# Performance work log

Measured on AMD Instinct MI355X. Metric: run time of the kernel, lower is better.

## Reference

```python
import jax, jax.numpy as jnp
import numpy as np

B_, T_, N_ = 32, 96, 68
IN_F, HID, GRU_H, NCLS = 3, 128, 128, 10
DEG = 8
N_NODES = B_ * T_ * N_
N_EDGES = N_NODES * DEG


def setup_inputs() -> dict:
    key = jax.random.key(0)
    ks = jax.random.split(key, 16)
    s = 0.05
    rn = lambda k, shp: (jax.random.normal(k, shp, jnp.float32) * s)
    return {
        "x": jax.random.normal(ks[0], (N_NODES, IN_F), jnp.float32),
        "edge_index": jax.random.randint(ks[1], (2, N_EDGES), 0, N_NODES, jnp.int32),
        "W_gcn0": rn(ks[2], (IN_F, HID)),
        "b_gcn0": jnp.zeros((HID,), jnp.float32),
        "W_gcn1": rn(ks[3], (HID, HID)),
        "b_gcn1": jnp.zeros((HID,), jnp.float32),
        "W_mlp": rn(ks[4], (HID, HID)),
        "b_mlp": jnp.zeros((HID,), jnp.float32),
        "W_ih": rn(ks[5], (3 * GRU_H, HID)),
        "W_hh": rn(ks[6], (3 * GRU_H, GRU_H)),
        "b_ih": jnp.zeros((3 * GRU_H,), jnp.float32),
        "b_hh": jnp.zeros((3 * GRU_H,), jnp.float32),
        "W_c1": rn(ks[7], (GRU_H, GRU_H // 2)),
        "b_c1": jnp.zeros((GRU_H // 2,), jnp.float32),
        "W_c2": rn(ks[8], (GRU_H // 2, NCLS)),
        "b_c2": jnp.zeros((NCLS,), jnp.float32),
        "B": B_, "T": T_, "N": N_,
    }


def reference(x, edge_index, W_gcn0, b_gcn0, W_gcn1, b_gcn1, W_mlp, b_mlp,
              W_ih, W_hh, b_ih, b_hh, W_c1, b_c1, W_c2, b_c2, B, T, N):
    n_nodes = x.shape[0]
    src, dst = edge_index[0], edge_index[1]
    # GCN degree with self-loops: deg[i] = 1 + in-degree(i)
    deg = jnp.ones((n_nodes,), x.dtype).at[dst].add(1.0)
    d_isqrt = jax.lax.rsqrt(deg)
    self_norm = (d_isqrt * d_isqrt)[:, None]  # self-loop norm = 1/deg
    edge_norm = (d_isqrt[src] * d_isqrt[dst])[:, None]

    def gcn(h, W, b):
        h = h @ W
        agg = jax.ops.segment_sum(h[src] * edge_norm, dst, num_segments=n_nodes)
        return agg + h * self_norm + b

    h = jax.nn.relu(gcn(x, W_gcn0, b_gcn0))
    h = jax.nn.relu(gcn(h, W_gcn1, b_gcn1))
    h = jax.nn.relu(h @ W_mlp + b_mlp)  # node_mlp (dropout off in eval)

    frames = h.reshape(B, T, N, -1).mean(axis=2)  # [B, T, HID] frame pooling

    def gru_step(hs, xt):
        gi = xt @ W_ih.T + b_ih
        gh = hs @ W_hh.T + b_hh
        ir, iz, inn = jnp.split(gi, 3, axis=-1)
        hr, hz, hn = jnp.split(gh, 3, axis=-1)
        r = jax.nn.sigmoid(ir + hr)
        z = jax.nn.sigmoid(iz + hz)
        n_new = jnp.tanh(inn + r * hn)
        return (1.0 - z) * n_new + z * hs, None

    h0 = jnp.zeros((B, GRU_H), frames.dtype)
    hT, _ = jax.lax.scan(gru_step, h0, jnp.swapaxes(frames, 0, 1))

    hidden = jax.nn.relu(hT @ W_c1 + b_c1)
    return hidden @ W_c2 + b_c2  # logits [B, num_classes]
```

## Files before the change

kernel.cpp:

```cpp
#include <hip/hip_runtime.h>

#define NN_TOT 208896
#define E_TOT  1671168
#define B_SZ   32
#define T_SZ   96
#define NPF    68
#define HID    128
#define NBINS  204
#define CAP    9216
#define NSB    816

typedef _Float16 f16x8 __attribute__((ext_vector_type(8)));
typedef _Float16 f16x2v __attribute__((ext_vector_type(2)));
typedef float f32x4 __attribute__((ext_vector_type(4)));

__global__ __launch_bounds__(256) void k_scatter(const int* __restrict__ src, const int* __restrict__ dst,
                                                 int* __restrict__ gcur, int2* __restrict__ er_tmp,
                                                 const float* __restrict__ Wih, const float* __restrict__ Whh,
                                                 const float* __restrict__ W1, const float* __restrict__ Wm,
                                                 const float* __restrict__ W0, const float* __restrict__ b0,
                                                 _Float16* __restrict__ Wihh, _Float16* __restrict__ Wihl,
                                                 _Float16* __restrict__ W1p, _Float16* __restrict__ Wmp,
                                                 _Float16* __restrict__ Whhp, _Float16* __restrict__ W0h,
                                                 _Float16* __restrict__ b0h) {
    const int bid = blockIdx.x;
    const int tid = threadIdx.x;
    if (bid >= NSB) {
        int i = (bid - NSB) * 256 + tid;
        {
            int e = i & 7;
            int lane = (i >> 3) & 63;
            int f = i >> 9;
            int j = f >> 2, kk = f & 3;
            int q = lane >> 4, p = lane & 15;
            float wv = Wih[(size_t)(j * 16 + p) * 128 + kk * 32 + q * 8 + e];
            _Float16 hi = (_Float16)wv;
            Wihh[i] = hi;
            Wihl[i] = (_Float16)(wv - (float)hi);
        }
        {
            int e = i & 7;
            int lane = (i >> 3) & 63;
            int f = i >> 9;
            int kk = f & 3, g = (f >> 2) % 3, wv = f / 12;
            int q = lane >> 4, c = lane & 15;
            Whhp[i] = (_Float16)Whh[(size_t)(g * 128 + 16 * wv + c) * 128 + kk * 32 + q * 8 + e];
        }
        if (i < 16384) {
            int f = i >> 9;
            int j = f >> 2, kk = f & 3;
            int lane = (i >> 3) & 63;
            int e = i & 7;
            int q = lane >> 4, p = lane & 15;
            int k = kk * 32 + q * 8 + e, n = j * 16 + p;
            W1p[i] = (_Float16)W1[k * 128 + n];
            Wmp[i] = (_Float16)Wm[k * 128 + n];
        }
        if (i < 384) W0h[i] = (_Float16)W0[i];
        if (i < 128) b0h[i] = (_Float16)b0[i];
        return;
    }
    __shared__ int hist[NBINS];
    __shared__ int lbase[NBINS];
    for (int i = tid; i < NBINS; i += 256) hist[i] = 0;
    __syncthreads();
    const int be = bid * 2048 + tid * 8;
    int s[8], d[8], rk[8];
    *(int4*)&s[0] = *(const int4*)&src[be];
    *(int4*)&s[4] = *(const int4*)&src[be + 4];
    *(int4*)&d[0] = *(const int4*)&dst[be];
    *(int4*)&d[4] = *(const int4*)&dst[be + 4];
#pragma unroll
    for (int j = 0; j < 8; ++j) rk[j] = atomicAdd(&hist[d[j] >> 10], 1);
    __syncthreads();
    for (int i = tid; i < NBINS; i += 256) lbase[i] = atomicAdd(&gcur[i], hist[i]);
    __syncthreads();
#pragma unroll
    for (int j = 0; j < 8; ++j) {
        int b = d[j] >> 10;
        er_tmp[(size_t)b * CAP + lbase[b] + rk[j]] = make_int2(s[j], d[j]);
    }
}

__global__ __launch_bounds__(256) void k_binsort2(const int2* __restrict__ er_tmp, const int* __restrict__ gcur,
                                                  const float* __restrict__ x, int* __restrict__ er,
                                                  int2* __restrict__ row2, float4* __restrict__ xd) {
    __shared__ int lcnt[1024];
    __shared__ int lofs[1024];
    __shared__ int ts[256];
    const int tid = threadIdx.x;
    const int nb = blockIdx.x << 10;
    const int base0 = blockIdx.x * CAP;
    for (int i = tid; i < 1024; i += 256) lcnt[i] = 0;
    __syncthreads();
    const int end = base0 + gcur[blockIdx.x];
    for (int e = base0 + tid; e < end; e += 256) {
        int2 ed = er_tmp[e];
        atomicAdd(&lcnt[ed.y - nb], 1);
    }
    __syncthreads();
    const int base = tid * 4;
    const int c0 = lcnt[base], c1 = lcnt[base + 1], c2 = lcnt[base + 2], c3 = lcnt[base + 3];
    int ssum = c0 + c1 + c2 + c3;
    ts[tid] = ssum;
    __syncthreads();
    int inc = ssum;
    for (int off = 1; off < 256; off <<= 1) {
        int add = (tid >= off) ? ts[tid - off] : 0;
        __syncthreads();
        inc += add;
        ts[tid] = inc;
        __syncthreads();
    }
    const int b0 = base0 + (inc - ssum);
    lofs[base] = b0;
    lofs[base + 1] = b0 + c0;
    lofs[base + 2] = b0 + c0 + c1;
    lofs[base + 3] = b0 + c0 + c1 + c2;
    row2[nb + base] = make_int2(b0, b0 + c0);
    row2[nb + base + 1] = make_int2(b0 + c0, b0 + c0 + c1);
    row2[nb + base + 2] = make_int2(b0 + c0 + c1, b0 + c0 + c1 + c2);
    row2[nb + base + 3] = make_int2(b0 + c0 + c1 + c2, b0 + ssum);
    {
        const float4* xv = (const float4*)(x + 3 * (size_t)(nb + base));
        float4 a = xv[0], b = xv[1], c = xv[2];
        float i0 = 1.0f / sqrtf(1.f + (float)c0);
        float i1 = 1.0f / sqrtf(1.f + (float)c1);
        float i2 = 1.0f / sqrtf(1.f + (float)c2);
        float i3 = 1.0f / sqrtf(1.f + (float)c3);
        xd[nb + base + 0] = make_float4(a.x * i0, a.y * i0, a.z * i0, i0);
        xd[nb + base + 1] = make_float4(a.w * i1, b.x * i1, b.y * i1, i1);
        xd[nb + base + 2] = make_float4(b.z * i2, b.w * i2, c.x * i2, i2);
        xd[nb + base + 3] = make_float4(c.y * i3, c.z * i3, c.w * i3, i3);
    }
    __syncthreads();
    for (int e = base0 + tid; e < end; e += 256) {
        int2 ed = er_tmp[e];
        int p = atomicAdd(&lofs[ed.y - nb], 1);
        er[p] = ed.x;
    }
}

__global__ __launch_bounds__(256) void k_z0(const float4* __restrict__ xd, const int2* __restrict__ row2,
                                            const int* __restrict__ er, float4* __restrict__ z0out) {
    const int tid = threadIdx.x;
    const int blk = blockIdx.x;
    const int li = tid >> 2;
    const int slot = tid & 3;
    const int n = blk * 64 + li;
    const int2 be2 = row2[n];
    float p0 = 0.f, p1 = 0.f, p2 = 0.f;
    for (int ei = be2.x + slot; ei < be2.y; ei += 4) {
        float4 f = xd[er[ei]];
        p0 += f.x;
        p1 += f.y;
        p2 += f.z;
    }
    p0 += __shfl_xor(p0, 1); p1 += __shfl_xor(p1, 1); p2 += __shfl_xor(p2, 1);
    p0 += __shfl_xor(p0, 2); p1 += __shfl_xor(p1, 2); p2 += __shfl_xor(p2, 2);
    if (slot == 0) {
        const float4 own = xd[n];
        const float w = own.w;
        float4 z;
        z.x = w * (p0 + own.x);
        z.y = w * (p1 + own.y);
        z.z = w * (p2 + own.z);
        z.w = w;
        z0out[n] = z;
    }
}

__global__ __launch_bounds__(256, 4) void k_agg_mm(const float4* __restrict__ z0, const int2* __restrict__ row2,
                                                   const int* __restrict__ er, const _Float16* __restrict__ W0h,
                                                   const _Float16* __restrict__ b0h, const _Float16* __restrict__ W1p,
                                                   const float* __restrict__ b1, _Float16* __restrict__ h1) {
    __shared__ __align__(16) _Float16 As[64 * 136];
    const int tid = threadIdx.x;
    const int w = tid >> 6, lane = tid & 63;
    const int blk = blockIdx.x;

    {
        const int node = blk * 64 + lane;
        const int2 be2 = row2[node];
        const int beg = be2.x, end = be2.y;
        const f16x2v* __restrict__ W0p = (const f16x2v*)W0h;
        const f16x2v* __restrict__ b0p = (const f16x2v*)b0h;
        const int pb = w * 16;
        const f16x2v zero2 = {(_Float16)0.f, (_Float16)0.f};
        f16x2v w0p[16], w1p[16], w2p[16], bbp[16];
#pragma unroll
        for (int j = 0; j < 16; ++j) {
            w0p[j] = W0p[pb + j];
            w1p[j] = W0p[64 + pb + j];
            w2p[j] = W0p[128 + pb + j];
            bbp[j] = b0p[pb + j];
        }
        const float4 zs = z0[node];
        const _Float16 isd = (_Float16)zs.w;
        const f16x2v dnn = {isd, isd};
        f16x2v accp[16];
        {
            _Float16 sx = (_Float16)zs.x, sy = (_Float16)zs.y, sz = (_Float16)zs.z;
            f16x2v zxx = {sx, sx}, zyy = {sy, sy}, zzz = {sz, sz};
#pragma unroll
            for (int j = 0; j < 16; ++j) {
                f16x2v t = zxx * w0p[j] + (zyy * w1p[j] + (zzz * w2p[j] + bbp[j]));
                t = __builtin_elementwise_max(t, zero2);
                accp[j] = t * dnn;
            }
        }
        int ei = beg;
        for (; ei + 2 <= end; ei += 2) {
            int sa = er[ei], sb = er[ei + 1];
            float4 za = z0[sa];
            float4 zb = z0[sb];
            _Float16 ax = (_Float16)za.x, ay = (_Float16)za.y, az = (_Float16)za.z;
            _Float16 aen = (_Float16)za.w;
            _Float16 bx = (_Float16)zb.x, by = (_Float16)zb.y, bz = (_Float16)zb.z;
            _Float16 ben = (_Float16)zb.w;
            f16x2v axx = {ax, ax}, ayy = {ay, ay}, azz = {az, az}, aee = {aen, aen};
            f16x2v bxx = {bx, bx}, byy = {by, by}, bzz = {bz, bz}, bee = {ben, ben};
#pragma unroll
            for (int j = 0; j < 16; ++j) {
                f16x2v t = axx * w0p[j] + (ayy * w1p[j] + (azz * w2p[j] + bbp[j]));
                t = __builtin_elementwise_max(t, zero2);
                accp[j] = t * aee + accp[j];
            }
#pragma unroll
            for (int j = 0; j < 16; ++j) {
                f16x2v t = bxx * w0p[j] + (byy * w1p[j] + (bzz * w2p[j] + bbp[j]));
                t = __builtin_elementwise_max(t, zero2);
                accp[j] = t * bee + accp[j];
            }
        }
        if (ei < end) {
            float4 za = z0[er[ei]];
            _Float16 ax = (_Float16)za.x, ay = (_Float16)za.y, az = (_Float16)za.z;
            _Float16 aen = (_Float16)za.w;
            f16x2v axx = {ax, ax}, ayy = {ay, ay}, azz = {az, az}, aee = {aen, aen};
#pragma unroll
            for (int j = 0; j < 16; ++j) {
                f16x2v t = axx * w0p[j] + (ayy * w1p[j] + (azz * w2p[j] + bbp[j]));
                t = __builtin_elementwise_max(t, zero2);
                accp[j] = t * aee + accp[j];
            }
        }
        _Float16* dst = &As[lane * 136 + w * 32];
#pragma unroll
        for (int j = 0; j < 16; ++j) *(f16x2v*)(dst + 2 * j) = accp[j] * dnn;
    }
    __syncthreads();

    const int q = lane >> 4, c = lane & 15;
    f16x8 afr[4];
#pragma unroll
    for (int kk = 0; kk < 4; ++kk) afr[kk] = *(const f16x8*)(&As[(w * 16 + c) * 136 + kk * 32 + q * 8]);
    const f16x8* __restrict__ Bv = (const f16x8*)W1p;
    _Float16* Cst = &As[w * 2176];
#pragma unroll
    for (int j = 0; j < 8; ++j) {
        f32x4 cc = {0.f, 0.f, 0.f, 0.f};
#pragma unroll
        for (int kk = 0; kk < 4; ++kk)
            cc = __builtin_amdgcn_mfma_f32_16x16x32_f16(afr[kk], Bv[(j * 4 + kk) * 64 + lane], cc, 0, 0, 0);
        const float bi = b1[j * 16 + c];
#pragma unroll
        for (int r = 0; r < 4; ++r) Cst[(q * 4 + r) * 128 + j * 16 + c] = (_Float16)fmaxf(cc[r] + bi, 0.f);
    }
#pragma unroll
    for (int it = 0; it < 4; ++it) {
        int idx = it * 64 + lane;
        *(f16x8*)(h1 + (size_t)(blk * 64 + w * 16) * 128 + idx * 8) = *(const f16x8*)(&As[w * 2176 + idx * 8]);
    }
}

__global__ __launch_bounds__(256) void k_mm_pool(const _Float16* __restrict__ h1, const _Float16* __restrict__ Wmp,
                                                 const float* __restrict__ bm, _Float16* __restrict__ FRh,
                                                 _Float16* __restrict__ FRl) {
    __shared__ __align__(16) _Float16 As[80 * 136];
    __shared__ float colpart[4 * 128];
    const int tid = threadIdx.x;
    const int w = tid >> 6, lane = tid & 63;
    const int q = lane >> 4, c = lane & 15;
    const int bt = blockIdx.x;

    const f16x8* __restrict__ srcv = (const f16x8*)(h1 + (size_t)bt * NPF * HID);
    for (int idx = tid; idx < 80 * 17; idx += 256) {
        int row = idx / 17, ch = idx % 17;
        f16x8 v;
        if (row < NPF && ch < 16) {
            v = srcv[row * 16 + ch];
        } else {
#pragma unroll
            for (int k = 0; k < 8; ++k) v[k] = (_Float16)0.f;
        }
        *(f16x8*)(&As[row * 136 + ch * 8]) = v;
    }
    __syncthreads();

    const f16x8* __restrict__ Bv = (const f16x8*)Wmp;
    const int npass = (w == 0) ? 2 : 1;
    for (int pass = 0; pass < npass; ++pass) {
        const int mt = pass ? 4 : w;
        f16x8 afr[4];
#pragma unroll
        for (int kk = 0; kk < 4; ++kk) afr[kk] = *(const f16x8*)(&As[(mt * 16 + c) * 136 + kk * 32 + q * 8]);
#pragma unroll
        for (int j = 0; j < 8; ++j) {
            f32x4 cc = {0.f, 0.f, 0.f, 0.f};
#pragma unroll
            for (int kk = 0; kk < 4; ++kk)
                cc = __builtin_amdgcn_mfma_f32_16x16x32_f16(afr[kk], Bv[(j * 4 + kk) * 64 + lane], cc, 0, 0, 0);
            const float bi = bm[j * 16 + c];
            float s = 0.f;
#pragma unroll
            for (int r = 0; r < 4; ++r) {
                int m = mt * 16 + q * 4 + r;
                float v = fmaxf(cc[r] + bi, 0.f);
                s += (m < NPF) ? v : 0.f;
            }
            s += __shfl_xor(s, 16);
            s += __shfl_xor(s, 32);
            if (lane < 16) {
                float* dst = &colpart[w * 128 + j * 16 + c];
                *dst = (pass == 0) ? s : (*dst + s);
            }
        }
    }
    __syncthreads();
    if (tid < 128) {
        float v = (colpart[tid] + colpart[128 + tid] + colpart[256 + tid] + colpart[384 + tid]) * (1.0f / NPF);
        _Float16 hi = (_Float16)v;
        FRh[(size_t)blockIdx.x * 128 + tid] = hi;
        FRl[(size_t)blockIdx.x * 128 + tid] = (_Float16)(v - (float)hi);
    }
}

__global__ __launch_bounds__(256) void k_gi(const _Float16* __restrict__ FRh, const _Float16* __restrict__ FRl,
                                            const _Float16* __restrict__ Wihh, const _Float16* __restrict__ Wihl,
                                            const float* __restrict__ bih, const float* __restrict__ bhh,
                                            float* __restrict__ GIt) {
    __shared__ __align__(16) _Float16 Ah[64 * 136];
    __shared__ __align__(16) _Float16 Al[64 * 136];
    const int tid = threadIdx.x;
    const int w = tid >> 6, lane = tid & 63;
    const int q = lane >> 4, p = lane & 15;
    const int nb = blockIdx.x * 64;

    const f16x8* __restrict__ sh = (const f16x8*)(FRh + (size_t)nb * 128);
    const f16x8* __restrict__ sl = (const f16x8*)(FRl + (size_t)nb * 128);
    for (int idx = tid; idx < 64 * 16; idx += 256) {
        int row = idx >> 4, ch = idx & 15;
        *(f16x8*)(&Ah[row * 136 + ch * 8]) = sh[idx];
        *(f16x8*)(&Al[row * 136 + ch * 8]) = sl[idx];
    }
    __syncthreads();

    f16x8 ah[4], al[4];
#pragma unroll
    for (int kk = 0; kk < 4; ++kk) {
        ah[kk] = *(const f16x8*)(&Ah[(w * 16 + p) * 136 + kk * 32 + q * 8]);
        al[kk] = *(const f16x8*)(&Al[(w * 16 + p) * 136 + kk * 32 + q * 8]);
    }
    const f16x8* __restrict__ Bh = (const f16x8*)Wihh;
    const f16x8* __restrict__ Bl = (const f16x8*)Wihl;
    int dr[4];
#pragma unroll
    for (int r = 0; r < 4; ++r) {
        int m = nb + w * 16 + q * 4 + r;
        int bb = m / 96, tt = m - bb * 96;
        dr[r] = (tt * B_SZ + bb) * 384;
    }
#pragma unroll
    for (int j = 0; j < 24; ++j) {
        f32x4 cc = {0.f, 0.f, 0.f, 0.f};
#pragma unroll
        for (int kk = 0; kk < 4; ++kk)
            cc = __builtin_amdgcn_mfma_f32_16x16x32_f16(ah[kk], Bh[(j * 4 + kk) * 64 + lane], cc, 0, 0, 0);
#pragma unroll
        for (int kk = 0; kk < 4; ++kk)
            cc = __builtin_amdgcn_mfma_f32_16x16x32_f16(ah[kk], Bl[(j * 4 + kk) * 64 + lane], cc, 0, 0, 0);
#pragma unroll
        for (int kk = 0; kk < 4; ++kk)
            cc = __builtin_amdgcn_mfma_f32_16x16x32_f16(al[kk], Bh[(j * 4 + kk) * 64 + lane], cc, 0, 0, 0);
        const int o = j * 16 + p;
        const float bias = bih[o] + ((o < 256) ? bhh[o] : 0.f);
        const float scale = (o < 256) ? -1.44269504f : 1.f;
#pragma unroll
        for (int r = 0; r < 4; ++r) GIt[dr[r] + o] = (cc[r] + bias) * scale;
    }
}

#define GRU_SYNC()                                              \
    asm volatile("s_waitcnt lgkmcnt(0)" ::: "memory");          \
    __builtin_amdgcn_s_barrier();                               \
    __builtin_amdgcn_sched_barrier(0);

#define GRU_BODY(PAR, GU, GL, JOFF)                                                                  \
    {                                                                                                \
        const _Float16* rb = hbuf[PAR];                                                              \
        _Float16* wb = hbuf[PAR ^ 1];                                                                \
        f16x8 afr[4];                                                                                \
        _Pragma("unroll") for (int kk = 0; kk < 4; ++kk)                                             \
            afr[kk] = *(const f16x8*)(&rb[c * 144 + kk * 32 + q * 8]);                               \
        const float* lp = pb + (size_t)(JOFF + 2) * STRIDE;                                          \
        _Pragma("unroll") for (int r = 0; r < 4; ++r)                                                \
            _Pragma("unroll") for (int g = 0; g < 3; ++g)                                            \
                GL[r * 3 + g] = lp[r * 384 + g * 128];                                               \
        f32x4 cc[3];                                                                                 \
        _Pragma("unroll") for (int g = 0; g < 3; ++g) {                                              \
            f32x4 a = {0.f, 0.f, 0.f, 0.f};                                                          \
            _Pragma("unroll") for (int kk = 0; kk < 4; ++kk)                                         \
                a = __builtin_amdgcn_mfma_f32_16x16x32_f16(afr[kk], bfr[g][kk], a, 0, 0, 0);         \
            cc[g] = a;                                                                               \
        }                                                                                            \
        _Pragma("unroll") for (int r = 0; r < 4; ++r) {                                              \
            float hn = cc[2][r] + bh2;                                                               \
            float rg = __builtin_amdgcn_rcpf(1.f + exp2f(fmaf(mL2E, cc[0][r], GU[r * 3 + 0])));      \
            float zg = __builtin_amdgcn_rcpf(1.f + exp2f(fmaf(mL2E, cc[1][r], GU[r * 3 + 1])));      \
            float arg = fmaf(rg, hn, GU[r * 3 + 2]);                                                 \
            float u = __builtin_amdgcn_rcpf(exp2f(2.f * L2E * arg) + 1.f);                           \
            float nn = fmaf(-2.f, u, 1.f);                                                           \
            h[r] = fmaf(zg, h[r] - nn, nn);                                                          \
            if (q < 2) wb[(q * 4 + r) * 144 + 16 * w + c] = (_Float16)h[r];                          \
        }                                                                                            \
        GRU_SYNC()                                                                                   \
    }

__global__ __launch_bounds__(512) __attribute__((amdgpu_waves_per_eu(1, 2)))
void k_gru(const float* __restrict__ GIt, const _Float16* __restrict__ Whhp,
           const float* __restrict__ bhh, float* __restrict__ hT) {
    __shared__ __align__(16) _Float16 hbuf[2][16 * 144];
    const int tid = threadIdx.x;
    const int w = tid >> 6, lane = tid & 63;
    const int q = lane >> 4, c = lane & 15;
    const int B = blockIdx.x;
    const float L2E = 1.44269504f;
    const float mL2E = -1.44269504f;
    const int STRIDE = B_SZ * 384;

    f16x8 bfr[3][4];
#pragma unroll
    for (int g = 0; g < 3; ++g)
#pragma unroll
        for (int kk = 0; kk < 4; ++kk)
            bfr[g][kk] = *(const f16x8*)(Whhp + (size_t)(((w * 3 + g) * 4 + kk) * 64 + lane) * 8);
    const float bh2 = bhh[256 + 16 * w + c];
    for (int i = tid; i < 2 * 16 * 144 / 2; i += 512) ((unsigned int*)hbuf)[i] = 0u;
    float h[4] = {0.f, 0.f, 0.f, 0.f};

    const int qq = (q < 2) ? q : 1;
    const float* pb = GIt + (size_t)(B * 8 + qq * 4) * 384 + 16 * w + c;
    float g0[12], g1[12], g2[12];
#pragma unroll
    for (int r = 0; r < 4; ++r)
#pragma unroll
        for (int g = 0; g < 3; ++g) {
            g0[r * 3 + g] = pb[r * 384 + g * 128];
            g1[r * 3 + g] = pb[STRIDE + r * 384 + g * 128];
        }
    GRU_SYNC()

    for (int it = 0; it < T_SZ / 6; ++it) {
        GRU_BODY(0, g0, g2, 0)
        GRU_BODY(1, g1, g0, 1)
        GRU_BODY(0, g2, g1, 2)
        GRU_BODY(1, g0, g2, 3)
        GRU_BODY(0, g1, g0, 4)
        GRU_BODY(1, g2, g1, 5)
        pb += 6 * (size_t)STRIDE;
    }
    if (q < 2) {
#pragma unroll
        for (int r = 0; r < 4; ++r) hT[(size_t)(B * 8 + q * 4 + r) * 128 + 16 * w + c] = h[r];
    }
}

__global__ __launch_bounds__(384) void k_cls(const float* __restrict__ hT, const float* __restrict__ Wc1,
                                             const float* __restrict__ bc1, const float* __restrict__ Wc2,
                                             const float* __restrict__ bc2, float* __restrict__ out) {
    __shared__ float hid[32 * 64];
    int tid = threadIdx.x;
    for (int idx = tid; idx < 2048; idx += 384) {
        int b = idx >> 6, j = idx & 63;
        float a = bc1[j];
#pragma unroll 8
        for (int k = 0; k < 128; ++k) a = fmaf(hT[b * 128 + k], Wc1[k * 64 + j], a);
        hid[idx] = fmaxf(a, 0.f);
    }
    __syncthreads();
    if (tid < 320) {
        int b = tid / 10, c = tid % 10;
        float a = bc2[c];
#pragma unroll 8
        for (int k = 0; k < 64; ++k) a = fmaf(hid[b * 64 + k], Wc2[k * 10 + c], a);
        out[tid] = a;
    }
}

extern "C" void kernel_launch(void* const* d_in, const int* in_sizes, int n_in, void* d_out, int out_size, void* d_ws,
                              size_t ws_size, hipStream_t stream) {
    const float* x = (const float*)d_in[0];
    const int* ei = (const int*)d_in[1];
    const int* e_src = ei;
    const int* e_dst = ei + E_TOT;
    const float* W0 = (const float*)d_in[2];
    const float* b0 = (const float*)d_in[3];
    const float* W1 = (const float*)d_in[4];
    const float* b1 = (const float*)d_in[5];
    const float* Wm = (const float*)d_in[6];
    const float* bm = (const float*)d_in[7];
    const float* Wih = (const float*)d_in[8];
    const float* Whh = (const float*)d_in[9];
    const float* bih = (const float*)d_in[10];
    const float* bhh = (const float*)d_in[11];
    const float* Wc1 = (const float*)d_in[12];
    const float* bc1 = (const float*)d_in[13];
    const float* Wc2 = (const float*)d_in[14];
    const float* bc2 = (const float*)d_in[15];
    float* out = (float*)d_out;

    char* base = (char*)d_ws;
    size_t off = 0;
    auto alloc = [&](size_t bytes) {
        size_t o = off;
        off = (off + bytes + 255) & ~(size_t)255;
        return o;
    };
    size_t o_gcur = alloc(256 * 4);
    size_t o_row2 = alloc((size_t)NN_TOT * 8);
    size_t o_er = alloc((size_t)NBINS * CAP * 4);
    size_t o_ertmp = alloc((size_t)NBINS * CAP * 8);
    size_t o_xd = alloc((size_t)NN_TOT * 16);
    size_t o_gi = alloc((size_t)(T_SZ + 2) * B_SZ * 384 * 4);
    size_t o_wihh = alloc((size_t)384 * 128 * 2);
    size_t o_wihl = alloc((size_t)384 * 128 * 2);
    size_t o_frh = alloc((size_t)B_SZ * T_SZ * 128 * 2);
    size_t o_frl = alloc((size_t)B_SZ * T_SZ * 128 * 2);
    size_t o_w1p = alloc((size_t)128 * 128 * 2);
    size_t o_wmp = alloc((size_t)128 * 128 * 2);
    size_t o_whhp = alloc((size_t)128 * 384 * 2);
    size_t o_w0h = alloc((size_t)384 * 2);
    size_t o_b0h = alloc((size_t)128 * 2);
    size_t o_ht = alloc((size_t)B_SZ * 128 * 4);
    size_t o_z0 = alloc((size_t)NN_TOT * 16);
    size_t o_h1 = alloc((size_t)NN_TOT * HID * 2);
    if (off > ws_size) return;

    int* gcur = (int*)(base + o_gcur);
    int2* row2 = (int2*)(base + o_row2);
    int* er = (int*)(base + o_er);
    int2* er_tmp = (int2*)(base + o_ertmp);
    float4* xd = (float4*)(base + o_xd);
    float* GIt = (float*)(base + o_gi);
    _Float16* Wihh = (_Float16*)(base + o_wihh);
    _Float16* Wihl = (_Float16*)(base + o_wihl);
    _Float16* FRh = (_Float16*)(base + o_frh);
    _Float16* FRl = (_Float16*)(base + o_frl);
    _Float16* W1p = (_Float16*)(base + o_w1p);
    _Float16* Wmp = (_Float16*)(base + o_wmp);
    _Float16* Whhp = (_Float16*)(base + o_whhp);
    _Float16* W0h = (_Float16*)(base + o_w0h);
    _Float16* b0h = (_Float16*)(base + o_b0h);
    float* hT = (float*)(base + o_ht);
    float4* z0 = (float4*)(base + o_z0);
    _Float16* h1 = (_Float16*)(base + o_h1);

    hipMemsetAsync(base + o_gcur, 0, 256 * 4, stream);

    k_scatter<<<NSB + 192, 256, 0, stream>>>(e_src, e_dst, gcur, er_tmp,
                                             Wih, Whh, W1, Wm, W0, b0,
                                             Wihh, Wihl, W1p, Wmp, Whhp, W0h, b0h);
    k_binsort2<<<NBINS, 256, 0, stream>>>(er_tmp, gcur, x, er, row2, xd);
    k_z0<<<NN_TOT / 64, 256, 0, stream>>>(xd, row2, er, z0);
    k_agg_mm<<<NN_TOT / 64, 256, 0, stream>>>(z0, row2, er, W0h, b0h, W1p, b1, h1);
    k_mm_pool<<<B_SZ * T_SZ, 256, 0, stream>>>(h1, Wmp, bm, FRh, FRl);
    k_gi<<<B_SZ * T_SZ / 64, 256, 0, stream>>>(FRh, FRl, Wihh, Wihl, bih, bhh, GIt);
    k_gru<<<4, 512, 0, stream>>>(GIt, Whhp, bhh, hT);
    k_cls<<<1, 384, 0, stream>>>(hT, Wc1, bc1, Wc2, bc2, out);
}
```

Measured before the change: 387.6 us.

## Pack edge records to 32-bit, register-cache bin records, fuse classifier into GRU

The intermediate edge records are packed into one int each: an 18-bit source plus a 10-bit local destination. This halves the er_tmp write and read traffic. The bin-sort kernel now loads each record once into a register array of 36 entries and reuses it for both the counting pass and the placement pass, instead of reading global memory twice. The classifier kernel is folded into the GRU kernel: a global ticket counter lets the last-finishing block run the MLP head, which removes one launch. This raises register pressure in binsort and depends on node ids fitting in 18 bits, bins holding at most 9216 records, and the ticket slot reusing gcur[255], which is zeroed by the existing memset.

```diff
diff --git a/kernel.cpp b/kernel.cpp
--- a/kernel.cpp
+++ b/kernel.cpp
@@ -15,7 +15,7 @@
 typedef float f32x4 __attribute__((ext_vector_type(4)));
 
 __global__ __launch_bounds__(256) void k_scatter(const int* __restrict__ src, const int* __restrict__ dst,
-                                                 int* __restrict__ gcur, int2* __restrict__ er_tmp,
+                                                 int* __restrict__ gcur, int* __restrict__ er_tmp,
                                                  const float* __restrict__ Wih, const float* __restrict__ Whh,
                                                  const float* __restrict__ W1, const float* __restrict__ Wm,
                                                  const float* __restrict__ W0, const float* __restrict__ b0,
@@ -78,11 +78,11 @@
 #pragma unroll
     for (int j = 0; j < 8; ++j) {
         int b = d[j] >> 10;
-        er_tmp[(size_t)b * CAP + lbase[b] + rk[j]] = make_int2(s[j], d[j]);
-    }
-}
-
-__global__ __launch_bounds__(256) void k_binsort2(const int2* __restrict__ er_tmp, const int* __restrict__ gcur,
+        er_tmp[(size_t)b * CAP + lbase[b] + rk[j]] = s[j] | ((d[j] & 1023) << 18);
+    }
+}
+
+__global__ __launch_bounds__(256) void k_binsort2(const int* __restrict__ er_tmp, const int* __restrict__ gcur,
                                                   const float* __restrict__ x, int* __restrict__ er,
                                                   int2* __restrict__ row2, float4* __restrict__ xd) {
     __shared__ int lcnt[1024];
@@ -93,11 +93,16 @@
     const int base0 = blockIdx.x * CAP;
     for (int i = tid; i < 1024; i += 256) lcnt[i] = 0;
     __syncthreads();
-    const int end = base0 + gcur[blockIdx.x];
-    for (int e = base0 + tid; e < end; e += 256) {
-        int2 ed = er_tmp[e];
-        atomicAdd(&lcnt[ed.y - nb], 1);
-    }
+    const int nrec = gcur[blockIdx.x];
+    int rec[36];
+#pragma unroll
+    for (int j = 0; j < 36; ++j) {
+        int idx = tid + j * 256;
+        rec[j] = (idx < nrec) ? er_tmp[base0 + idx] : -1;
+    }
+#pragma unroll
+    for (int j = 0; j < 36; ++j)
+        if (rec[j] >= 0) atomicAdd(&lcnt[rec[j] >> 18], 1);
     __syncthreads();
     const int base = tid * 4;
     const int c0 = lcnt[base], c1 = lcnt[base + 1], c2 = lcnt[base + 2], c3 = lcnt[base + 3];
@@ -134,11 +139,12 @@
         xd[nb + base + 3] = make_float4(c.y * i3, c.z * i3, c.w * i3, i3);
     }
     __syncthreads();
-    for (int e = base0 + tid; e < end; e += 256) {
-        int2 ed = er_tmp[e];
-        int p = atomicAdd(&lofs[ed.y - nb], 1);
-        er[p] = ed.x;
-    }
+#pragma unroll
+    for (int j = 0; j < 36; ++j)
+        if (rec[j] >= 0) {
+            int p = atomicAdd(&lofs[rec[j] >> 18], 1);
+            er[p] = rec[j] & 0x3FFFF;
+        }
 }
 
 __global__ __launch_bounds__(256) void k_z0(const float4* __restrict__ xd, const int2* __restrict__ row2,
@@ -429,8 +435,12 @@
 
 __global__ __launch_bounds__(512) __attribute__((amdgpu_waves_per_eu(1, 2)))
 void k_gru(const float* __restrict__ GIt, const _Float16* __restrict__ Whhp,
-           const float* __restrict__ bhh, float* __restrict__ hT) {
+           const float* __restrict__ bhh, float* __restrict__ hT,
+           const float* __restrict__ Wc1, const float* __restrict__ bc1,
+           const float* __restrict__ Wc2, const float* __restrict__ bc2,
+           float* __restrict__ out, int* __restrict__ ticket) {
     __shared__ __align__(16) _Float16 hbuf[2][16 * 144];
+    __shared__ int tick;
     const int tid = threadIdx.x;
     const int w = tid >> 6, lane = tid & 63;
     const int q = lane >> 4, c = lane & 15;
@@ -474,27 +484,30 @@
 #pragma unroll
         for (int r = 0; r < 4; ++r) hT[(size_t)(B * 8 + q * 4 + r) * 128 + 16 * w + c] = h[r];
     }
-}
-
-__global__ __launch_bounds__(384) void k_cls(const float* __restrict__ hT, const float* __restrict__ Wc1,
-                                             const float* __restrict__ bc1, const float* __restrict__ Wc2,
-                                             const float* __restrict__ bc2, float* __restrict__ out) {
-    __shared__ float hid[32 * 64];
-    int tid = threadIdx.x;
-    for (int idx = tid; idx < 2048; idx += 384) {
-        int b = idx >> 6, j = idx & 63;
-        float a = bc1[j];
+
+    __syncthreads();
+    __threadfence();
+    __syncthreads();
+    if (tid == 0) tick = atomicAdd(ticket, 1);
+    __syncthreads();
+    if (tick == 3) {
+        __threadfence();
+        float* hid = (float*)hbuf;
+        for (int idx = tid; idx < 2048; idx += 512) {
+            int b = idx >> 6, j = idx & 63;
+            float a = bc1[j];
 #pragma unroll 8
-        for (int k = 0; k < 128; ++k) a = fmaf(hT[b * 128 + k], Wc1[k * 64 + j], a);
-        hid[idx] = fmaxf(a, 0.f);
-    }
-    __syncthreads();
-    if (tid < 320) {
-        int b = tid / 10, c = tid % 10;
-        float a = bc2[c];
+            for (int k = 0; k < 128; ++k) a = fmaf(hT[b * 128 + k], Wc1[k * 64 + j], a);
+            hid[idx] = fmaxf(a, 0.f);
+        }
+        __syncthreads();
+        if (tid < 320) {
+            int b = tid / 10, cc2 = tid % 10;
+            float a = bc2[cc2];
 #pragma unroll 8
-        for (int k = 0; k < 64; ++k) a = fmaf(hid[b * 64 + k], Wc2[k * 10 + c], a);
-        out[tid] = a;
+            for (int k = 0; k < 64; ++k) a = fmaf(hid[b * 64 + k], Wc2[k * 10 + cc2], a);
+            out[tid] = a;
+        }
     }
 }
 
@@ -530,7 +543,7 @@
     size_t o_gcur = alloc(256 * 4);
     size_t o_row2 = alloc((size_t)NN_TOT * 8);
     size_t o_er = alloc((size_t)NBINS * CAP * 4);
-    size_t o_ertmp = alloc((size_t)NBINS * CAP * 8);
+    size_t o_ertmp = alloc((size_t)NBINS * CAP * 4);
     size_t o_xd = alloc((size_t)NN_TOT * 16);
     size_t o_gi = alloc((size_t)(T_SZ + 2) * B_SZ * 384 * 4);
     size_t o_wihh = alloc((size_t)384 * 128 * 2);
@@ -548,9 +561,10 @@
     if (off > ws_size) return;
 
     int* gcur = (int*)(base + o_gcur);
+    int* ticket = gcur + 255;
     int2* row2 = (int2*)(base + o_row2);
     int* er = (int*)(base + o_er);
-    int2* er_tmp = (int2*)(base + o_ertmp);
+    int* er_tmp = (int*)(base + o_ertmp);
     float4* xd = (float4*)(base + o_xd);
     float* GIt = (float*)(base + o_gi);
     _Float16* Wihh = (_Float16*)(base + o_wihh);
@@ -576,6 +590,5 @@
     k_agg_mm<<<NN_TOT / 64, 256, 0, stream>>>(z0, row2, er, W0h, b0h, W1p, b1, h1);
     k_mm_pool<<<B_SZ * T_SZ, 256, 0, stream>>>(h1, Wmp, bm, FRh, FRl);
     k_gi<<<B_SZ * T_SZ / 64, 256, 0, stream>>>(FRh, FRl, Wihh, Wihl, bih, bhh, GIt);
-    k_gru<<<4, 512, 0, stream>>>(GIt, Whhp, bhh, hT);
-    k_cls<<<1, 384, 0, stream>>>(hT, Wc1, bc1, Wc2, bc2, out);
-}
+    k_gru<<<4, 512, 0, stream>>>(GIt, Whhp, bhh, hT, Wc1, bc1, Wc2, bc2, out, ticket);
+}
```

New measurement: 377.5 us. 1.03x faster.
